# Performance work log

Hardware: AMD Instinct MI355X
Metric: run time of the kernel (lower is better)

## Reference

```python
import jax, jax.numpy as jnp
import numpy as np

T, B, H, O = 512, 64, 512, 128
G = 4 * H  # PyTorch gate order: i, f, g, o


def setup_inputs() -> dict:
    key = jax.random.key(0)
    ks = jax.random.split(key, 10)
    s = 1.0 / np.sqrt(H)
    return {
        "x": jax.random.normal(ks[0], (T, B, H), jnp.float32),
        "h0": jnp.zeros((1, B, H), jnp.float32),
        "c0": jnp.zeros((1, B, H), jnp.float32),
        "W_ih1": jax.random.normal(ks[1], (G, H), jnp.float32) * s,
        "W_hh1": jax.random.normal(ks[2], (G, H), jnp.float32) * s,
        "b_ih1": jax.random.normal(ks[3], (G,), jnp.float32) * s,
        "b_hh1": jax.random.normal(ks[4], (G,), jnp.float32) * s,
        "W_ih2": jax.random.normal(ks[5], (G, H), jnp.float32) * s,
        "W_hh2": jax.random.normal(ks[6], (G, H), jnp.float32) * s,
        "b_ih2": jax.random.normal(ks[7], (G,), jnp.float32) * s,
        "b_hh2": jax.random.normal(ks[8], (G,), jnp.float32) * s,
        "W_out": jax.random.normal(ks[9], (O, H), jnp.float32) * s,
        "b_out": jnp.zeros((O,), jnp.float32),
    }


def _lstm_layer(x, h0, c0, W_ih, W_hh, b_ih, b_hh):
    # x: [T,B,H]; h0,c0: [B,H]. PyTorch LSTM math, gate order i,f,g,o.
    xg = jnp.einsum('tbh,gh->tbg', x, W_ih) + b_ih + b_hh  # [T,B,4H]
    W_hh_T = W_hh.T

    def step(carry, xg_t):
        h, c = carry
        g = xg_t + h @ W_hh_T
        i, f, gc, o = jnp.split(g, 4, axis=-1)
        i = jax.nn.sigmoid(i)
        f = jax.nn.sigmoid(f)
        gc = jnp.tanh(gc)
        o = jax.nn.sigmoid(o)
        c = f * c + i * gc
        h = o * jnp.tanh(c)
        return (h, c), h

    (hT, cT), ys = jax.lax.scan(step, (h0, c0), xg)
    return ys, hT, cT


def reference(x, h0, c0, W_ih1, W_hh1, b_ih1, b_hh1, W_ih2, W_hh2, b_ih2, b_hh2, W_out, b_out):
    y1, h1, c1 = _lstm_layer(x, h0[0], c0[0], W_ih1, W_hh1, b_ih1, b_hh1)
    # Faithful quirk: lstm2 is initialized with lstm1's FINAL (h, c).
    y2, h2, c2 = _lstm_layer(y1, h1, c1, W_ih2, W_hh2, b_ih2, b_hh2)
    out = y2[-1] @ W_out.T + b_out  # Linear on last timestep; LogSoftmax is unused in forward
    return out, h2[None], c2[None]
```

## Files before the change

kernel.cpp:

```cpp
#include <hip/hip_runtime.h>

typedef unsigned short u16;
typedef unsigned int u32;
typedef unsigned long long u64;
using f32x4 = __attribute__((ext_vector_type(4))) float;
using s16x8 = __attribute__((ext_vector_type(8))) short;
using u32x4 = __attribute__((ext_vector_type(4))) unsigned int;
using u64x2 = __attribute__((ext_vector_type(2))) unsigned long long;

constexpr int Tn = 512, Bn = 64, Hn = 512, Gn = 2048, On = 128;
constexpr int NS = 16;
constexpr int NG = 4;

constexpr size_t HT_BYTES = (size_t)(Tn + 1) * Bn * Hn * 2;
constexpr size_t XG_BYTES = (size_t)Tn * (size_t)Gn * Bn * 2;
constexpr size_t WB_BYTES = (size_t)Gn * Hn * 2;
constexpr size_t OFF_CMID = 0;
constexpr size_t OFF_HMID = OFF_CMID + (size_t)Bn * Hn * 4;
constexpr size_t OFF_WB1  = OFF_HMID + (size_t)Bn * Hn * 4;
constexpr size_t OFF_WB2  = OFF_WB1 + WB_BYTES;
constexpr size_t OFF_HT1  = OFF_WB2 + WB_BYTES;
constexpr size_t OFF_XG   = OFF_HT1 + HT_BYTES;

__device__ __forceinline__ u16 f2b(float f) {
  union { float f; unsigned u; } v; v.f = f;
  unsigned r = v.u + 0x7fffu + ((v.u >> 16) & 1u);
  return (u16)(r >> 16);
}
__device__ __forceinline__ float b2f(u16 u) {
  union { unsigned u; float f; } v; v.u = ((unsigned)u) << 16; return v.f;
}
__device__ __forceinline__ s16x8 pack8(float4 lo, float4 hi) {
  s16x8 r;
  r[0] = (short)f2b(lo.x); r[1] = (short)f2b(lo.y); r[2] = (short)f2b(lo.z); r[3] = (short)f2b(lo.w);
  r[4] = (short)f2b(hi.x); r[5] = (short)f2b(hi.y); r[6] = (short)f2b(hi.z); r[7] = (short)f2b(hi.w);
  return r;
}
__device__ __forceinline__ float sigm(float x) {
  float e = __builtin_amdgcn_exp2f(-1.4426950408889634f * x);
  return __builtin_amdgcn_rcpf(1.0f + e);
}
__device__ __forceinline__ float tanh_(float x) {
  float e = __builtin_amdgcn_exp2f(-2.885390081777927f * x);
  return __builtin_amdgcn_rcpf(1.0f + e) * 2.0f - 1.0f;
}
__device__ __forceinline__ u64 ld64_sc(const u64* p) {
  return __hip_atomic_load(p, __ATOMIC_RELAXED, __HIP_MEMORY_SCOPE_AGENT);
}
__device__ __forceinline__ void st64_sc(u64* p, u64 v) {
  __hip_atomic_store(p, v, __ATOMIC_RELAXED, __HIP_MEMORY_SCOPE_AGENT);
}
__device__ __forceinline__ ushort4 u64_to_us4(u64 q) { union { u64 q; ushort4 v; } u; u.q = q; return u.v; }
__device__ __forceinline__ s16x8 u32x4_to_s16x8(u32x4 a) { union { u32x4 a; s16x8 v; } u; u.a = a; return u.v; }

__global__ __launch_bounds__(256)
void cvt_kernel(const float* __restrict__ in, u16* __restrict__ out, int n4) {
  const int i = blockIdx.x * 256 + threadIdx.x;
  if (i < n4) {
    float4 v = ((const float4*)in)[i];
    ushort4 o; o.x = f2b(v.x); o.y = f2b(v.y); o.z = f2b(v.z); o.w = f2b(v.w);
    ((ushort4*)out)[i] = o;
  }
}

template<bool AF32>
__device__ __forceinline__ void proj_core(
    const int wg, const int nwg, const void* __restrict__ Ap,
    const u16* __restrict__ Wb, const float* __restrict__ bih,
    const float* __restrict__ bhh, u16* __restrict__ xg)
{
  const int lane = threadIdx.x & 63, wave = threadIdx.x >> 6;
  const int lrow = lane & 15, lk8 = (lane >> 4) << 3;
  for (int tile = wg; tile < 4096; tile += nwg) {
    const int m0 = (tile >> 4) * 128 + (wave & 1) * 64;
    const int n0 = (tile & 15) * 128 + (wave >> 1) * 64;
    f32x4 acc[4][4] = {};
    for (int ks = 0; ks < 16; ++ks) {
      const int k0 = ks * 32 + lk8;
      s16x8 af[4], bfr[4];
      if constexpr (AF32) {
#pragma unroll
        for (int mt = 0; mt < 4; ++mt) {
          const float* ap = (const float*)Ap + (size_t)(m0 + mt * 16 + lrow) * Hn + k0;
          float4 lo = *(const float4*)ap, hi = *(const float4*)(ap + 4);
          af[mt] = pack8(lo, hi);
        }
      } else {
        u32x4 a4[4];
        const char* pa0 = (const char*)((const u16*)Ap + (size_t)(m0 + 0 * 16 + lrow) * Hn + k0);
        const char* pa1 = (const char*)((const u16*)Ap + (size_t)(m0 + 1 * 16 + lrow) * Hn + k0);
        const char* pa2 = (const char*)((const u16*)Ap + (size_t)(m0 + 2 * 16 + lrow) * Hn + k0);
        const char* pa3 = (const char*)((const u16*)Ap + (size_t)(m0 + 3 * 16 + lrow) * Hn + k0);
        asm volatile("global_load_dwordx4 %0, %1, off sc1" : "=v"(a4[0]) : "v"(pa0) : "memory");
        asm volatile("global_load_dwordx4 %0, %1, off sc1" : "=v"(a4[1]) : "v"(pa1) : "memory");
        asm volatile("global_load_dwordx4 %0, %1, off sc1" : "=v"(a4[2]) : "v"(pa2) : "memory");
        asm volatile("global_load_dwordx4 %0, %1, off sc1" : "=v"(a4[3]) : "v"(pa3) : "memory");
        asm volatile("s_waitcnt vmcnt(0)" ::: "memory");
        while (true) {
          bool bad = false;
#pragma unroll
          for (int mt = 0; mt < 4; ++mt)
#pragma unroll
            for (int d = 0; d < 4; ++d) bad = bad | (a4[mt][d] == 0xFFFFFFFFu);
          if (!bad) break;
          __builtin_amdgcn_s_sleep(8);
          asm volatile("global_load_dwordx4 %0, %1, off sc1" : "=v"(a4[0]) : "v"(pa0) : "memory");
          asm volatile("global_load_dwordx4 %0, %1, off sc1" : "=v"(a4[1]) : "v"(pa1) : "memory");
          asm volatile("global_load_dwordx4 %0, %1, off sc1" : "=v"(a4[2]) : "v"(pa2) : "memory");
          asm volatile("global_load_dwordx4 %0, %1, off sc1" : "=v"(a4[3]) : "v"(pa3) : "memory");
          asm volatile("s_waitcnt vmcnt(0)" ::: "memory");
        }
#pragma unroll
        for (int mt = 0; mt < 4; ++mt) af[mt] = u32x4_to_s16x8(a4[mt]);
      }
#pragma unroll
      for (int nt = 0; nt < 4; ++nt)
        bfr[nt] = *(const s16x8*)(Wb + (size_t)(n0 + nt * 16 + lrow) * Hn + k0);
#pragma unroll
      for (int mt = 0; mt < 4; ++mt)
#pragma unroll
        for (int nt = 0; nt < 4; ++nt)
          acc[mt][nt] = __builtin_amdgcn_mfma_f32_16x16x32_bf16(af[mt], bfr[nt], acc[mt][nt], 0, 0, 0);
    }
    const int rbase = (lane >> 4) << 2;
#pragma unroll
    for (int nt = 0; nt < 4; ++nt) {
      const int n = n0 + nt * 16 + lrow;
      const float bias = bih[n] + bhh[n];
#pragma unroll
      for (int mt = 0; mt < 4; ++mt) {
        const int m = m0 + mt * 16 + rbase;
        const int t = m >> 6, b = m & 63;
        const u64 pv = (u64)f2b(acc[mt][nt][0] + bias)
                     | ((u64)f2b(acc[mt][nt][1] + bias) << 16)
                     | ((u64)f2b(acc[mt][nt][2] + bias) << 32)
                     | ((u64)f2b(acc[mt][nt][3] + bias) << 48);
        st64_sc((u64*)(xg + ((size_t)t * Gn + n) * Bn + b), pv);
      }
    }
  }
}

template<bool POLL_XG>
__device__ __forceinline__ void scan_core(
    const int wgid, const u16* __restrict__ xg, const float* __restrict__ Whh,
    const float* __restrict__ hinit, const float* __restrict__ cinit,
    u16* __restrict__ ht, float* __restrict__ h_fin, float* __restrict__ c_fin)
{
  const int g = wgid >> 4, s = wgid & (NS - 1);
  const int tid = threadIdx.x;
  const int lane = tid & 63, w = tid >> 6;
  const int x16 = lane & 15, grp = lane >> 4;
  const int jj = x16 & 7;
  const int j0 = s * 32 + w * 8;
  const int brow = g * 16;
  const int bth = brow + grp * 4;

  __shared__ char hlds[16 * 1024];
  __shared__ u16 hstage[2][16][32];

  const size_t grow0 = (size_t)(x16 >> 3) * Hn + j0 + jj;
  const size_t grow1 = (size_t)(2 + (x16 >> 3)) * Hn + j0 + jj;
  s16x8 bwh[2][16];
#pragma unroll
  for (int nt = 0; nt < 2; ++nt) {
    const size_t grow = nt ? grow1 : grow0;
#pragma unroll
    for (int ks = 0; ks < 16; ++ks) {
      const float* wp = Whh + grow * Hn + ks * 32 + grp * 8;
      float4 lo = *(const float4*)wp, hi = *(const float4*)(wp + 4);
      bwh[nt][ks] = pack8(lo, hi);
    }
  }

  float c[4];
#pragma unroll
  for (int r = 0; r < 4; ++r) c[r] = cinit[(size_t)(bth + r) * Hn + j0 + jj];

  if (tid < 128) {
    const int row = tid >> 3, cq = tid & 7;
    const float* hp = hinit + (size_t)(brow + row) * Hn + s * 32 + cq * 4;
    u64 v = (u64)f2b(hp[0]) | ((u64)f2b(hp[1]) << 16)
          | ((u64)f2b(hp[2]) << 32) | ((u64)f2b(hp[3]) << 48);
    st64_sc((u64*)(ht + (size_t)(brow + row) * Hn + s * 32 + cq * 4), v);
  }

  ushort4 xv0, xv1;
  {
    const u16* xa = xg + grow0 * Bn + bth;
    const u16* xb = xg + grow1 * Bn + bth;
    if constexpr (POLL_XG) {
      u64 a = ld64_sc((const u64*)xa), b = ld64_sc((const u64*)xb);
      while (a == ~0ull || b == ~0ull) {
        __builtin_amdgcn_s_sleep(2);
        if (a == ~0ull) a = ld64_sc((const u64*)xa);
        if (b == ~0ull) b = ld64_sc((const u64*)xb);
      }
      xv0 = u64_to_us4(a); xv1 = u64_to_us4(b);
    } else {
      xv0 = *(const ushort4*)xa; xv1 = *(const ushort4*)xb;
    }
  }

  for (int t = 0; t < Tn; ++t) {
    const u16* rt = ht + (size_t)t * Bn * Hn;
    const u64* p0 = (const u64*)(rt + (size_t)(brow + (tid >> 6)) * Hn) + ((tid & 63) << 1);
    u64 v[8];
#pragma unroll
    for (int i = 0; i < 4; ++i) {
      v[2 * i]     = ld64_sc(p0 + i * 512);
      v[2 * i + 1] = ld64_sc(p0 + i * 512 + 1);
    }
    while (true) {
      bool all = true;
#pragma unroll
      for (int i = 0; i < 8; ++i) all = all && (v[i] != ~0ull);
      if (all) break;
      __builtin_amdgcn_s_sleep(1);
#pragma unroll
      for (int i = 0; i < 4; ++i) {
        if (v[2 * i]     == ~0ull) v[2 * i]     = ld64_sc(p0 + i * 512);
        if (v[2 * i + 1] == ~0ull) v[2 * i + 1] = ld64_sc(p0 + i * 512 + 1);
      }
    }
    {
      const int row = tid >> 6, ci = tid & 63;
#pragma unroll
      for (int i = 0; i < 4; ++i) {
        const int rr = row + 4 * i;
        u64x2 q; q[0] = v[2 * i]; q[1] = v[2 * i + 1];
        *(u64x2*)(hlds + rr * 1024 + ((ci ^ (rr & 7)) * 16)) = q;
      }
    }
    __syncthreads();
    f32x4 acc0, acc1;
    acc0[0] = b2f(xv0.x); acc0[1] = b2f(xv0.y); acc0[2] = b2f(xv0.z); acc0[3] = b2f(xv0.w);
    acc1[0] = b2f(xv1.x); acc1[1] = b2f(xv1.y); acc1[2] = b2f(xv1.z); acc1[3] = b2f(xv1.w);
#pragma unroll
    for (int ks = 0; ks < 16; ++ks) {
      const s16x8 a = *(const s16x8*)(hlds + x16 * 1024 + ((((ks << 2) + grp) ^ jj) * 16));
      acc0 = __builtin_amdgcn_mfma_f32_16x16x32_bf16(a, bwh[0][ks], acc0, 0, 0, 0);
      acc1 = __builtin_amdgcn_mfma_f32_16x16x32_bf16(a, bwh[1][ks], acc1, 0, 0, 0);
    }
    float hv[4];
#pragma unroll
    for (int r = 0; r < 4; ++r) {
      const float p0v = acc0[r], p1v = acc1[r];
      const float q0 = __shfl_xor(p0v, 8, 64);
      const float q1 = __shfl_xor(p1v, 8, 64);
      const bool lo = (x16 < 8);
      const float gi = lo ? p0v : q0;
      const float gf = lo ? q0 : p0v;
      const float gg = lo ? p1v : q1;
      const float go = lo ? q1 : p1v;
      const float cn = sigm(gf) * c[r] + sigm(gi) * tanh_(gg);
      c[r] = cn;
      hv[r] = sigm(go) * tanh_(cn);
    }
    if (t == Tn - 1 && x16 < 8) {
#pragma unroll
      for (int r = 0; r < 4; ++r) {
        h_fin[(size_t)(bth + r) * Hn + j0 + jj] = hv[r];
        c_fin[(size_t)(bth + r) * Hn + j0 + jj] = c[r];
      }
    }
    {
      float a0 = hv[0], a1 = hv[1], a2 = hv[2], a3 = hv[3];
      const int p = x16 & 3;
      float tvu;
      tvu = (p & 1) ? a0 : a1;  tvu = __shfl_xor(tvu, 1, 64);
      if (p & 1) a0 = tvu; else a1 = tvu;
      tvu = (p & 1) ? a2 : a3;  tvu = __shfl_xor(tvu, 1, 64);
      if (p & 1) a2 = tvu; else a3 = tvu;
      tvu = (p & 2) ? a0 : a2;  tvu = __shfl_xor(tvu, 2, 64);
      if (p & 2) a0 = tvu; else a2 = tvu;
      tvu = (p & 2) ? a1 : a3;  tvu = __shfl_xor(tvu, 2, 64);
      if (p & 2) a1 = tvu; else a3 = tvu;
      if (x16 < 8) {
        const int cc = (x16 >> 2) & 1;
        const u64 yv = (u64)f2b(a0) | ((u64)f2b(a1) << 16)
                     | ((u64)f2b(a2) << 32) | ((u64)f2b(a3) << 48);
        *(u64*)&hstage[t & 1][grp * 4 + p][w * 8 + cc * 4] = yv;
      }
    }
    __syncthreads();
    if (!(tid & 1)) {
      const int q = tid >> 1, row = q >> 3, cq = q & 7;
      const u64 yv = *(const u64*)&hstage[t & 1][row][cq * 4];
      st64_sc((u64*)(ht + (size_t)(t + 1) * Bn * Hn + (size_t)(brow + row) * Hn + s * 32 + cq * 4), yv);
    }
    const int tn2 = (t + 1 < Tn) ? t + 1 : t;
    {
      const u16* xa = xg + ((size_t)tn2 * Gn + grow0) * Bn + bth;
      const u16* xb = xg + ((size_t)tn2 * Gn + grow1) * Bn + bth;
      if constexpr (POLL_XG) {
        u64 a = ld64_sc((const u64*)xa), b = ld64_sc((const u64*)xb);
        while (a == ~0ull || b == ~0ull) {
          __builtin_amdgcn_s_sleep(2);
          if (a == ~0ull) a = ld64_sc((const u64*)xa);
          if (b == ~0ull) b = ld64_sc((const u64*)xb);
        }
        xv0 = u64_to_us4(a); xv1 = u64_to_us4(b);
      } else {
        xv0 = *(const ushort4*)xa; xv1 = *(const ushort4*)xb;
      }
    }
  }
}

__global__ __launch_bounds__(256, 1)
void mega_full(const float* __restrict__ x,
               const u16* __restrict__ Wb1, const float* __restrict__ bih1, const float* __restrict__ bhh1,
               const float* __restrict__ Whh1, const float* __restrict__ h0, const float* __restrict__ c0,
               u16* __restrict__ ht1, u16* __restrict__ xg,
               const u16* __restrict__ Wb2, const float* __restrict__ bih2, const float* __restrict__ bhh2,
               float* __restrict__ h_mid, float* __restrict__ c_mid)
{
  const int bid = blockIdx.x;
  if (bid < 64)
    scan_core<true>(bid, xg, Whh1, h0, c0, ht1, h_mid, c_mid);
  else if (bid < 160)
    proj_core<true>(bid - 64, 96, x, Wb1, bih1, bhh1, xg);
  else
    proj_core<false>(bid - 160, 96, ht1 + (size_t)Bn * Hn, Wb2, bih2, bhh2, xg);
}

__global__ __launch_bounds__(256, 1)
void scan_plain(const u16* __restrict__ xg, const float* __restrict__ Whh,
                const float* __restrict__ hinit, const float* __restrict__ cinit,
                u16* __restrict__ ht, float* __restrict__ h_fin, float* __restrict__ c_fin)
{
  scan_core<false>(blockIdx.x, xg, Whh, hinit, cinit, ht, h_fin, c_fin);
}

__global__ __launch_bounds__(128)
void out_kernel(const float* __restrict__ h2, const float* __restrict__ Wout,
                const float* __restrict__ bout, float* __restrict__ out)
{
  const int b = blockIdx.x, o = threadIdx.x;
  const float4* hp = (const float4*)(h2 + (size_t)b * Hn);
  const float4* wp = (const float4*)(Wout + (size_t)o * Hn);
  float acc = 0.f;
#pragma unroll 4
  for (int k = 0; k < Hn / 4; ++k) {
    float4 h4 = hp[k], w4 = wp[k];
    acc += h4.x * w4.x + h4.y * w4.y + h4.z * w4.z + h4.w * w4.w;
  }
  out[(size_t)b * On + o] = acc + bout[o];
}

extern "C" void kernel_launch(void* const* d_in, const int* in_sizes, int n_in,
                              void* d_out, int out_size, void* d_ws, size_t ws_size,
                              hipStream_t stream) {
  const float* x     = (const float*)d_in[0];
  const float* h0    = (const float*)d_in[1];
  const float* c0    = (const float*)d_in[2];
  const float* W_ih1 = (const float*)d_in[3];
  const float* W_hh1 = (const float*)d_in[4];
  const float* b_ih1 = (const float*)d_in[5];
  const float* b_hh1 = (const float*)d_in[6];
  const float* W_ih2 = (const float*)d_in[7];
  const float* W_hh2 = (const float*)d_in[8];
  const float* b_ih2 = (const float*)d_in[9];
  const float* b_hh2 = (const float*)d_in[10];
  const float* W_out = (const float*)d_in[11];
  const float* b_out = (const float*)d_in[12];

  float* out    = (float*)d_out;
  float* h2_out = out + (size_t)Bn * On;
  float* c2_out = h2_out + (size_t)Bn * Hn;

  char* w = (char*)d_ws;
  float* c_mid = (float*)(w + OFF_CMID);
  float* h_mid = (float*)(w + OFF_HMID);
  u16*   Wb1   = (u16*)(w + OFF_WB1);
  u16*   Wb2   = (u16*)(w + OFF_WB2);
  u16*   ht1   = (u16*)(w + OFF_HT1);
  u16*   xg    = (u16*)(w + OFF_XG);

  const int nw4 = Gn * Hn / 4;

  hipMemsetAsync(ht1, 0xFF, HT_BYTES, stream);
  hipMemsetAsync(xg, 0xFF, XG_BYTES, stream);
  cvt_kernel<<<(nw4 + 255) / 256, 256, 0, stream>>>(W_ih1, Wb1, nw4);
  cvt_kernel<<<(nw4 + 255) / 256, 256, 0, stream>>>(W_ih2, Wb2, nw4);

  mega_full<<<256, 256, 0, stream>>>(x, Wb1, b_ih1, b_hh1, W_hh1, h0, c0,
                                     ht1, xg, Wb2, b_ih2, b_hh2, h_mid, c_mid);
  hipMemsetAsync(ht1, 0xFF, HT_BYTES, stream);
  scan_plain<<<NG * NS, 256, 0, stream>>>(xg, W_hh2, h_mid, c_mid, ht1, h2_out, c2_out);
  out_kernel<<<Bn, 128, 0, stream>>>(h2_out, W_out, b_out, out);
}
```

Baseline: 2.619 ms.

## Halve scan workgroups by processing two batch groups per workgroup

Each recurrent-scan workgroup now handles two 16-row batch groups in sequence, reusing the same register-resident W_hh fragments, so only 32 scan workgroups are needed instead of 64. The freed workgroups in the fused kernel go to the input-projection producers, which rise from 96 to 112 per layer. This cuts the number of workgroups polling and synchronising per timestep, at the cost of a longer serial critical path per step, since each workgroup runs two dependent step bodies back to back.

```diff
diff --git a/kernel.cpp b/kernel.cpp
--- a/kernel.cpp
+++ b/kernel.cpp
@@ -10,7 +10,7 @@
 
 constexpr int Tn = 512, Bn = 64, Hn = 512, Gn = 2048, On = 128;
 constexpr int NS = 16;
-constexpr int NG = 4;
+constexpr int NSCAN = 32;
 
 constexpr size_t HT_BYTES = (size_t)(Tn + 1) * Bn * Hn * 2;
 constexpr size_t XG_BYTES = (size_t)Tn * (size_t)Gn * Bn * 2;
@@ -142,53 +142,106 @@
 }
 
 template<bool POLL_XG>
-__device__ __forceinline__ void scan_core(
-    const int wgid, const u16* __restrict__ xg, const float* __restrict__ Whh,
-    const float* __restrict__ hinit, const float* __restrict__ cinit,
-    u16* __restrict__ ht, float* __restrict__ h_fin, float* __restrict__ c_fin)
-{
-  const int g = wgid >> 4, s = wgid & (NS - 1);
-  const int tid = threadIdx.x;
-  const int lane = tid & 63, w = tid >> 6;
-  const int x16 = lane & 15, grp = lane >> 4;
-  const int jj = x16 & 7;
-  const int j0 = s * 32 + w * 8;
-  const int brow = g * 16;
-  const int bth = brow + grp * 4;
-
-  __shared__ char hlds[16 * 1024];
-  __shared__ u16 hstage[2][16][32];
-
-  const size_t grow0 = (size_t)(x16 >> 3) * Hn + j0 + jj;
-  const size_t grow1 = (size_t)(2 + (x16 >> 3)) * Hn + j0 + jj;
-  s16x8 bwh[2][16];
-#pragma unroll
-  for (int nt = 0; nt < 2; ++nt) {
-    const size_t grow = nt ? grow1 : grow0;
-#pragma unroll
-    for (int ks = 0; ks < 16; ++ks) {
-      const float* wp = Whh + grow * Hn + ks * 32 + grp * 8;
-      float4 lo = *(const float4*)wp, hi = *(const float4*)(wp + 4);
-      bwh[nt][ks] = pack8(lo, hi);
-    }
-  }
-
-  float c[4];
-#pragma unroll
-  for (int r = 0; r < 4; ++r) c[r] = cinit[(size_t)(bth + r) * Hn + j0 + jj];
-
-  if (tid < 128) {
-    const int row = tid >> 3, cq = tid & 7;
-    const float* hp = hinit + (size_t)(brow + row) * Hn + s * 32 + cq * 4;
-    u64 v = (u64)f2b(hp[0]) | ((u64)f2b(hp[1]) << 16)
-          | ((u64)f2b(hp[2]) << 32) | ((u64)f2b(hp[3]) << 48);
-    st64_sc((u64*)(ht + (size_t)(brow + row) * Hn + s * 32 + cq * 4), v);
-  }
-
-  ushort4 xv0, xv1;
+__device__ __forceinline__ void scan_step(
+    const int t, const int tid, const int x16, const int grp, const int jj,
+    const int j0, const int w, const int brow, const int bth,
+    const size_t grow0, const size_t grow1,
+    const s16x8 (&bwh)[2][16],
+    char* __restrict__ hlds, u16 (* __restrict__ hstage)[16][32],
+    const u16* __restrict__ xg, u16* __restrict__ ht,
+    float* __restrict__ h_fin, float* __restrict__ c_fin,
+    float* __restrict__ c, ushort4& xv0, ushort4& xv1)
+{
+  const u16* rt = ht + (size_t)t * Bn * Hn;
+  const u64* p0 = (const u64*)(rt + (size_t)(brow + (tid >> 6)) * Hn) + ((tid & 63) << 1);
+  u64 v[8];
+#pragma unroll
+  for (int i = 0; i < 4; ++i) {
+    v[2 * i]     = ld64_sc(p0 + i * 512);
+    v[2 * i + 1] = ld64_sc(p0 + i * 512 + 1);
+  }
+  while (true) {
+    bool all = true;
+#pragma unroll
+    for (int i = 0; i < 8; ++i) all = all && (v[i] != ~0ull);
+    if (all) break;
+    __builtin_amdgcn_s_sleep(1);
+#pragma unroll
+    for (int i = 0; i < 4; ++i) {
+      if (v[2 * i]     == ~0ull) v[2 * i]     = ld64_sc(p0 + i * 512);
+      if (v[2 * i + 1] == ~0ull) v[2 * i + 1] = ld64_sc(p0 + i * 512 + 1);
+    }
+  }
   {
-    const u16* xa = xg + grow0 * Bn + bth;
-    const u16* xb = xg + grow1 * Bn + bth;
+    const int row = tid >> 6, ci = tid & 63;
+#pragma unroll
+    for (int i = 0; i < 4; ++i) {
+      const int rr = row + 4 * i;
+      u64x2 q; q[0] = v[2 * i]; q[1] = v[2 * i + 1];
+      *(u64x2*)(hlds + rr * 1024 + ((ci ^ (rr & 7)) * 16)) = q;
+    }
+  }
+  __syncthreads();
+  f32x4 acc0, acc1;
+  acc0[0] = b2f(xv0.x); acc0[1] = b2f(xv0.y); acc0[2] = b2f(xv0.z); acc0[3] = b2f(xv0.w);
+  acc1[0] = b2f(xv1.x); acc1[1] = b2f(xv1.y); acc1[2] = b2f(xv1.z); acc1[3] = b2f(xv1.w);
+#pragma unroll
+  for (int ks = 0; ks < 16; ++ks) {
+    const s16x8 a = *(const s16x8*)(hlds + x16 * 1024 + ((((ks << 2) + grp) ^ jj) * 16));
+    acc0 = __builtin_amdgcn_mfma_f32_16x16x32_bf16(a, bwh[0][ks], acc0, 0, 0, 0);
+    acc1 = __builtin_amdgcn_mfma_f32_16x16x32_bf16(a, bwh[1][ks], acc1, 0, 0, 0);
+  }
+  float hv[4];
+#pragma unroll
+  for (int r = 0; r < 4; ++r) {
+    const float p0v = acc0[r], p1v = acc1[r];
+    const float q0 = __shfl_xor(p0v, 8, 64);
+    const float q1 = __shfl_xor(p1v, 8, 64);
+    const bool lo = (x16 < 8);
+    const float gi = lo ? p0v : q0;
+    const float gf = lo ? q0 : p0v;
+    const float gg = lo ? p1v : q1;
+    const float go = lo ? q1 : p1v;
+    const float cn = sigm(gf) * c[r] + sigm(gi) * tanh_(gg);
+    c[r] = cn;
+    hv[r] = sigm(go) * tanh_(cn);
+  }
+  if (t == Tn - 1 && x16 < 8) {
+#pragma unroll
+    for (int r = 0; r < 4; ++r) {
+      h_fin[(size_t)(bth + r) * Hn + j0 + jj] = hv[r];
+      c_fin[(size_t)(bth + r) * Hn + j0 + jj] = c[r];
+    }
+  }
+  {
+    float a0 = hv[0], a1 = hv[1], a2 = hv[2], a3 = hv[3];
+    const int p = x16 & 3;
+    float tvu;
+    tvu = (p & 1) ? a0 : a1;  tvu = __shfl_xor(tvu, 1, 64);
+    if (p & 1) a0 = tvu; else a1 = tvu;
+    tvu = (p & 1) ? a2 : a3;  tvu = __shfl_xor(tvu, 1, 64);
+    if (p & 1) a2 = tvu; else a3 = tvu;
+    tvu = (p & 2) ? a0 : a2;  tvu = __shfl_xor(tvu, 2, 64);
+    if (p & 2) a0 = tvu; else a2 = tvu;
+    tvu = (p & 2) ? a1 : a3;  tvu = __shfl_xor(tvu, 2, 64);
+    if (p & 2) a1 = tvu; else a3 = tvu;
+    if (x16 < 8) {
+      const int cc = (x16 >> 2) & 1;
+      const u64 yv = (u64)f2b(a0) | ((u64)f2b(a1) << 16)
+                   | ((u64)f2b(a2) << 32) | ((u64)f2b(a3) << 48);
+      *(u64*)&hstage[t & 1][grp * 4 + p][w * 8 + cc * 4] = yv;
+    }
+  }
+  __syncthreads();
+  if (!(tid & 1)) {
+    const int q = tid >> 1, row = q >> 3, cq = q & 7;
+    const u64 yv = *(const u64*)&hstage[t & 1][row][cq * 4];
+    st64_sc((u64*)(ht + (size_t)(t + 1) * Bn * Hn + (size_t)(brow + row) * Hn + (j0 - w * 8) + cq * 4), yv);
+  }
+  const int tn2 = (t + 1 < Tn) ? t + 1 : t;
+  {
+    const u16* xa = xg + ((size_t)tn2 * Gn + grow0) * Bn + bth;
+    const u16* xb = xg + ((size_t)tn2 * Gn + grow1) * Bn + bth;
     if constexpr (POLL_XG) {
       u64 a = ld64_sc((const u64*)xa), b = ld64_sc((const u64*)xb);
       while (a == ~0ull || b == ~0ull) {
@@ -201,110 +254,85 @@
       xv0 = *(const ushort4*)xa; xv1 = *(const ushort4*)xb;
     }
   }
+}
+
+template<bool POLL_XG>
+__device__ __forceinline__ void scan2_core(
+    const int wgid, const u16* __restrict__ xg, const float* __restrict__ Whh,
+    const float* __restrict__ hinit, const float* __restrict__ cinit,
+    u16* __restrict__ ht, float* __restrict__ h_fin, float* __restrict__ c_fin)
+{
+  const int a = wgid >> 4, s = wgid & (NS - 1);
+  const int tid = threadIdx.x;
+  const int lane = tid & 63, w = tid >> 6;
+  const int x16 = lane & 15, grp = lane >> 4;
+  const int jj = x16 & 7;
+  const int j0 = s * 32 + w * 8;
+  const int browA = (2 * a) * 16, browB = (2 * a + 1) * 16;
+  const int bthA = browA + grp * 4, bthB = browB + grp * 4;
+
+  __shared__ char hlds[2][16 * 1024];
+  __shared__ u16 hstage[2][2][16][32];
+
+  const size_t grow0 = (size_t)(x16 >> 3) * Hn + j0 + jj;
+  const size_t grow1 = (size_t)(2 + (x16 >> 3)) * Hn + j0 + jj;
+  s16x8 bwh[2][16];
+#pragma unroll
+  for (int nt = 0; nt < 2; ++nt) {
+    const size_t grow = nt ? grow1 : grow0;
+#pragma unroll
+    for (int ks = 0; ks < 16; ++ks) {
+      const float* wp = Whh + grow * Hn + ks * 32 + grp * 8;
+      float4 lo = *(const float4*)wp, hi = *(const float4*)(wp + 4);
+      bwh[nt][ks] = pack8(lo, hi);
+    }
+  }
+
+  float cA[4], cB[4];
+#pragma unroll
+  for (int r = 0; r < 4; ++r) {
+    cA[r] = cinit[(size_t)(bthA + r) * Hn + j0 + jj];
+    cB[r] = cinit[(size_t)(bthB + r) * Hn + j0 + jj];
+  }
+
+  if (tid < 128) {
+    const int row = tid >> 3, cq = tid & 7;
+#pragma unroll
+    for (int ga = 0; ga < 2; ++ga) {
+      const int br = ga ? browB : browA;
+      const float* hp = hinit + (size_t)(br + row) * Hn + s * 32 + cq * 4;
+      u64 v = (u64)f2b(hp[0]) | ((u64)f2b(hp[1]) << 16)
+            | ((u64)f2b(hp[2]) << 32) | ((u64)f2b(hp[3]) << 48);
+      st64_sc((u64*)(ht + (size_t)(br + row) * Hn + s * 32 + cq * 4), v);
+    }
+  }
+
+  ushort4 xvA0, xvA1, xvB0, xvB1;
+#pragma unroll
+  for (int ga = 0; ga < 2; ++ga) {
+    const int bt = ga ? bthB : bthA;
+    const u16* xa = xg + grow0 * Bn + bt;
+    const u16* xb = xg + grow1 * Bn + bt;
+    ushort4 r0, r1;
+    if constexpr (POLL_XG) {
+      u64 p = ld64_sc((const u64*)xa), q = ld64_sc((const u64*)xb);
+      while (p == ~0ull || q == ~0ull) {
+        __builtin_amdgcn_s_sleep(2);
+        if (p == ~0ull) p = ld64_sc((const u64*)xa);
+        if (q == ~0ull) q = ld64_sc((const u64*)xb);
+      }
+      r0 = u64_to_us4(p); r1 = u64_to_us4(q);
+    } else {
+      r0 = *(const ushort4*)xa; r1 = *(const ushort4*)xb;
+    }
+    if (ga) { xvB0 = r0; xvB1 = r1; } else { xvA0 = r0; xvA1 = r1; }
+  }
 
   for (int t = 0; t < Tn; ++t) {
-    const u16* rt = ht + (size_t)t * Bn * Hn;
-    const u64* p0 = (const u64*)(rt + (size_t)(brow + (tid >> 6)) * Hn) + ((tid & 63) << 1);
-    u64 v[8];
-#pragma unroll
-    for (int i = 0; i < 4; ++i) {
-      v[2 * i]     = ld64_sc(p0 + i * 512);
-      v[2 * i + 1] = ld64_sc(p0 + i * 512 + 1);
-    }
-    while (true) {
-      bool all = true;
-#pragma unroll
-      for (int i = 0; i < 8; ++i) all = all && (v[i] != ~0ull);
-      if (all) break;
-      __builtin_amdgcn_s_sleep(1);
-#pragma unroll
-      for (int i = 0; i < 4; ++i) {
-        if (v[2 * i]     == ~0ull) v[2 * i]     = ld64_sc(p0 + i * 512);
-        if (v[2 * i + 1] == ~0ull) v[2 * i + 1] = ld64_sc(p0 + i * 512 + 1);
-      }
-    }
-    {
-      const int row = tid >> 6, ci = tid & 63;
-#pragma unroll
-      for (int i = 0; i < 4; ++i) {
-        const int rr = row + 4 * i;
-        u64x2 q; q[0] = v[2 * i]; q[1] = v[2 * i + 1];
-        *(u64x2*)(hlds + rr * 1024 + ((ci ^ (rr & 7)) * 16)) = q;
-      }
-    }
-    __syncthreads();
-    f32x4 acc0, acc1;
-    acc0[0] = b2f(xv0.x); acc0[1] = b2f(xv0.y); acc0[2] = b2f(xv0.z); acc0[3] = b2f(xv0.w);
-    acc1[0] = b2f(xv1.x); acc1[1] = b2f(xv1.y); acc1[2] = b2f(xv1.z); acc1[3] = b2f(xv1.w);
-#pragma unroll
-    for (int ks = 0; ks < 16; ++ks) {
-      const s16x8 a = *(const s16x8*)(hlds + x16 * 1024 + ((((ks << 2) + grp) ^ jj) * 16));
-      acc0 = __builtin_amdgcn_mfma_f32_16x16x32_bf16(a, bwh[0][ks], acc0, 0, 0, 0);
-      acc1 = __builtin_amdgcn_mfma_f32_16x16x32_bf16(a, bwh[1][ks], acc1, 0, 0, 0);
-    }
-    float hv[4];
-#pragma unroll
-    for (int r = 0; r < 4; ++r) {
-      const float p0v = acc0[r], p1v = acc1[r];
-      const float q0 = __shfl_xor(p0v, 8, 64);
-      const float q1 = __shfl_xor(p1v, 8, 64);
-      const bool lo = (x16 < 8);
-      const float gi = lo ? p0v : q0;
-      const float gf = lo ? q0 : p0v;
-      const float gg = lo ? p1v : q1;
-      const float go = lo ? q1 : p1v;
-      const float cn = sigm(gf) * c[r] + sigm(gi) * tanh_(gg);
-      c[r] = cn;
-      hv[r] = sigm(go) * tanh_(cn);
-    }
-    if (t == Tn - 1 && x16 < 8) {
-#pragma unroll
-      for (int r = 0; r < 4; ++r) {
-        h_fin[(size_t)(bth + r) * Hn + j0 + jj] = hv[r];
-        c_fin[(size_t)(bth + r) * Hn + j0 + jj] = c[r];
-      }
-    }
-    {
-      float a0 = hv[0], a1 = hv[1], a2 = hv[2], a3 = hv[3];
-      const int p = x16 & 3;
-      float tvu;
-      tvu = (p & 1) ? a0 : a1;  tvu = __shfl_xor(tvu, 1, 64);
-      if (p & 1) a0 = tvu; else a1 = tvu;
-      tvu = (p & 1) ? a2 : a3;  tvu = __shfl_xor(tvu, 1, 64);
-      if (p & 1) a2 = tvu; else a3 = tvu;
-      tvu = (p & 2) ? a0 : a2;  tvu = __shfl_xor(tvu, 2, 64);
-      if (p & 2) a0 = tvu; else a2 = tvu;
-      tvu = (p & 2) ? a1 : a3;  tvu = __shfl_xor(tvu, 2, 64);
-      if (p & 2) a1 = tvu; else a3 = tvu;
-      if (x16 < 8) {
-        const int cc = (x16 >> 2) & 1;
-        const u64 yv = (u64)f2b(a0) | ((u64)f2b(a1) << 16)
-                     | ((u64)f2b(a2) << 32) | ((u64)f2b(a3) << 48);
-        *(u64*)&hstage[t & 1][grp * 4 + p][w * 8 + cc * 4] = yv;
-      }
-    }
-    __syncthreads();
-    if (!(tid & 1)) {
-      const int q = tid >> 1, row = q >> 3, cq = q & 7;
-      const u64 yv = *(const u64*)&hstage[t & 1][row][cq * 4];
-      st64_sc((u64*)(ht + (size_t)(t + 1) * Bn * Hn + (size_t)(brow + row) * Hn + s * 32 + cq * 4), yv);
-    }
-    const int tn2 = (t + 1 < Tn) ? t + 1 : t;
-    {
-      const u16* xa = xg + ((size_t)tn2 * Gn + grow0) * Bn + bth;
-      const u16* xb = xg + ((size_t)tn2 * Gn + grow1) * Bn + bth;
-      if constexpr (POLL_XG) {
-        u64 a = ld64_sc((const u64*)xa), b = ld64_sc((const u64*)xb);
-        while (a == ~0ull || b == ~0ull) {
-          __builtin_amdgcn_s_sleep(2);
-          if (a == ~0ull) a = ld64_sc((const u64*)xa);
-          if (b == ~0ull) b = ld64_sc((const u64*)xb);
-        }
-        xv0 = u64_to_us4(a); xv1 = u64_to_us4(b);
-      } else {
-        xv0 = *(const ushort4*)xa; xv1 = *(const ushort4*)xb;
-      }
-    }
+    scan_step<POLL_XG>(t, tid, x16, grp, jj, j0, w, browA, bthA, grow0, grow1,
+                       bwh, hlds[0], hstage[0], xg, ht, h_fin, c_fin, cA, xvA0, xvA1);
+    scan_step<POLL_XG>(t, tid, x16, grp, jj, j0, w, browB, bthB, grow0, grow1,
+                       bwh, hlds[1], hstage[1], xg, ht, h_fin, c_fin, cB, xvB0, xvB1);
   }
 }
 
@@ -317,12 +345,12 @@
                float* __restrict__ h_mid, float* __restrict__ c_mid)
 {
   const int bid = blockIdx.x;
-  if (bid < 64)
-    scan_core<true>(bid, xg, Whh1, h0, c0, ht1, h_mid, c_mid);
-  else if (bid < 160)
-    proj_core<true>(bid - 64, 96, x, Wb1, bih1, bhh1, xg);
+  if (bid < NSCAN)
+    scan2_core<true>(bid, xg, Whh1, h0, c0, ht1, h_mid, c_mid);
+  else if (bid < 144)
+    proj_core<true>(bid - NSCAN, 112, x, Wb1, bih1, bhh1, xg);
   else
-    proj_core<false>(bid - 160, 96, ht1 + (size_t)Bn * Hn, Wb2, bih2, bhh2, xg);
+    proj_core<false>(bid - 144, 112, ht1 + (size_t)Bn * Hn, Wb2, bih2, bhh2, xg);
 }
 
 __global__ __launch_bounds__(256, 1)
@@ -330,7 +358,7 @@
                 const float* __restrict__ hinit, const float* __restrict__ cinit,
                 u16* __restrict__ ht, float* __restrict__ h_fin, float* __restrict__ c_fin)
 {
-  scan_core<false>(blockIdx.x, xg, Whh, hinit, cinit, ht, h_fin, c_fin);
+  scan2_core<false>(blockIdx.x, xg, Whh, hinit, cinit, ht, h_fin, c_fin);
 }
 
 __global__ __launch_bounds__(128)
@@ -388,6 +416,6 @@
   mega_full<<<256, 256, 0, stream>>>(x, Wb1, b_ih1, b_hh1, W_hh1, h0, c0,
                                      ht1, xg, Wb2, b_ih2, b_hh2, h_mid, c_mid);
   hipMemsetAsync(ht1, 0xFF, HT_BYTES, stream);
-  scan_plain<<<NG * NS, 256, 0, stream>>>(xg, W_hh2, h_mid, c_mid, ht1, h2_out, c2_out);
+  scan_plain<<<NSCAN, 256, 0, stream>>>(xg, W_hh2, h_mid, c_mid, ht1, h2_out, c2_out);
   out_kernel<<<Bn, 128, 0, stream>>>(h2_out, W_out, b_out, out);
 }
```

After: 4.628 ms. 76.7% more time.
